# Kernel tuning notes

Hardware: AMD Instinct MI355X
Metric: run time of the kernel (lower is better)

## Reference

```python
import jax, jax.numpy as jnp
import numpy as np

BLOCK_SIZE = 16
MASK_TOKEN_ID = 31999
D_MODEL = 2048
N_HEADS = 16
VOCAB = 32000
NEG = -1e30


def setup_inputs() -> dict:
    key = jax.random.key(0)
    ks = jax.random.split(key, 8)
    B, S, D, V = 1, 1024, D_MODEL, VOCAB
    sd = 1.0 / np.sqrt(D)
    return {
        "input_ids": jax.random.randint(ks[0], (B, S), 0, V),
        "attention_mask": jnp.ones((B, S), dtype=jnp.float32),
        "hidden_states": jax.random.normal(ks[1], (B, S, D), dtype=jnp.float32),
        "loss_mask": jnp.ones((B, S), dtype=jnp.float32),
        "embed_table": jax.random.normal(ks[2], (V, D), dtype=jnp.float32) * 0.02,
        "Wq": jax.random.normal(ks[3], (D, D), dtype=jnp.float32) * sd,
        "Wk": jax.random.normal(ks[4], (D, D), dtype=jnp.float32) * sd,
        "Wv": jax.random.normal(ks[5], (D, D), dtype=jnp.float32) * sd,
        "Wo": jax.random.normal(ks[6], (D, D), dtype=jnp.float32) * sd,
        "lm_head_w": jax.random.normal(ks[7], (D, V), dtype=jnp.float32) * sd,
    }


def reference(input_ids, attention_mask, hidden_states, loss_mask,
              embed_table, Wq, Wk, Wv, Wo, lm_head_w):
    B, S = input_ids.shape
    bs = BLOCK_SIZE
    L = (S // bs) * bs  # effective_len
    input_ids = input_ids[:, :L]
    hidden_states = hidden_states[:, :L, :]
    loss_mask = loss_mask[:, :L]

    positions = jnp.arange(L)
    is_block_start = positions % bs == 0
    block_ids = positions // bs

    # noise input: first token of each block real, rest MASK
    noise_ids = jnp.where(is_block_start[None, :], input_ids, MASK_TOKEN_ID)
    noise_emb = embed_table[noise_ids]  # [B, L, D]

    # [L, 2L] DFlash mask: ctx kv visible if its block < q block; noise kv if same block
    ctx_vis = block_ids[None, :] < block_ids[:, None]
    noise_vis = block_ids[:, None] == block_ids[None, :]
    full_mask = jnp.concatenate([ctx_vis, noise_vis], axis=1)  # [L, 2L] bool

    # draft attention: q from noise tokens, kv over [target_hidden ; noise]
    H = N_HEADS
    hd = hidden_states.shape[-1] // H
    kv_in = jnp.concatenate([hidden_states, noise_emb], axis=1)  # [B, 2L, D]
    q = (noise_emb @ Wq).reshape(B, L, H, hd).transpose(0, 2, 1, 3)      # [B,H,L,hd]
    k = (kv_in @ Wk).reshape(B, 2 * L, H, hd).transpose(0, 2, 1, 3)      # [B,H,2L,hd]
    v = (kv_in @ Wv).reshape(B, 2 * L, H, hd).transpose(0, 2, 1, 3)
    scores = jnp.einsum("bhqd,bhkd->bhqk", q, k) / jnp.sqrt(jnp.float32(hd))
    scores = jnp.where(full_mask[None, None, :, :], scores, NEG)
    attn = jax.nn.softmax(scores, axis=-1)
    ctx = jnp.einsum("bhqk,bhkd->bhqd", attn, v)
    hidden = ctx.transpose(0, 2, 1, 3).reshape(B, L, -1) @ Wo  # [B, L, D]

    logits = hidden @ lm_head_w  # [B, L, V]

    # dflash loss mask: exclude first block and block starts (gamma=None)
    is_first_block = block_ids == 0
    valid = (~is_first_block) & (~is_block_start)
    combined = loss_mask * valid.astype(jnp.float32)  # [B, L]
    active = combined > 1e-6

    logp = jax.nn.log_softmax(logits, axis=-1)
    ce = -jnp.take_along_axis(logp, input_ids[..., None], axis=-1)[..., 0]  # [B, L]
    count = jnp.sum(active.astype(jnp.float32))
    loss = jnp.sum(jnp.where(active, ce, 0.0)) / count

    preds = jnp.argmax(logits, axis=-1)
    correct = jnp.sum(jnp.where(active, (preds == input_ids).astype(jnp.float32), 0.0))
    accuracy = correct / count
    return loss, accuracy
```

## Files before the change

### kernel.cpp

```cpp
#include <hip/hip_runtime.h>

typedef unsigned int uint32;
typedef unsigned short u16;
typedef __attribute__((ext_vector_type(8))) short bf16x8;
typedef __attribute__((ext_vector_type(4))) float f32x4;

__device__ __forceinline__ u16 f2b(float f) {
  uint32 u = __float_as_uint(f);
  u = (u + 0x7fffu + ((u >> 16) & 1u)) >> 16;
  return (u16)u;
}
__device__ __forceinline__ float b2f(u16 h) {
  return __uint_as_float(((uint32)h) << 16);
}
__device__ __forceinline__ void gl_lds16(const void* g, void* l) {
  typedef const __attribute__((address_space(1))) void* gp_t;
  typedef __attribute__((address_space(3))) void* lp_t;
  __builtin_amdgcn_global_load_lds((gp_t)g, (lp_t)l, 16, 0, 0);
}

#define L 1024
#define D 2048
#define NH 16
#define HD 128
#define VOCAB 32000
#define KV 2048
#define MASK_ID 31999

static constexpr long OFF_KV  = 0;
static constexpr long OFF_WTQ = OFF_KV  + 8388608;
static constexpr long OFF_WTK = OFF_WTQ + 8388608;
static constexpr long OFF_WTV = OFF_WTK + 8388608;
static constexpr long OFF_WTO = OFF_WTV + 8388608;
static constexpr long OFF_Q   = OFF_WTO + 8388608;
static constexpr long OFF_K   = OFF_Q   + 4194304;
static constexpr long OFF_VT  = OFF_K   + 8388608;
static constexpr long OFF_SC  = OFF_VT  + 8388608;
static constexpr long OFF_CTX = OFF_SC  + 67108864;
static constexpr long OFF_HID = OFF_CTX + 4194304;
static constexpr long OFF_LMT = OFF_HID + 4194304;
static constexpr long OFF_LOG = OFF_LMT + 131072000;
static constexpr long OFF_ROW = OFF_LOG + 65536000;
static constexpr long WS_NEED = OFF_ROW + 8192;

__global__ __launch_bounds__(256) void prep_kv(const float* __restrict__ hs,
                                               const int* __restrict__ ids,
                                               const float* __restrict__ emb,
                                               u16* __restrict__ kv) {
  int r = blockIdx.x;
  int t = threadIdx.x;
  const float* src;
  if (r < L) {
    src = hs + (long)r * D;
  } else {
    int p = r - L;
    int id = ((p & 15) == 0) ? ids[p] : MASK_ID;
    src = emb + (long)id * D;
  }
  float4 a = *(const float4*)(src + t * 8);
  float4 b = *(const float4*)(src + t * 8 + 4);
  u16* dst = kv + (long)r * D + t * 8;
  ushort4 o0, o1;
  o0.x = f2b(a.x); o0.y = f2b(a.y); o0.z = f2b(a.z); o0.w = f2b(a.w);
  o1.x = f2b(b.x); o1.y = f2b(b.y); o1.z = f2b(b.z); o1.w = f2b(b.w);
  *(ushort4*)dst = o0;
  *(ushort4*)(dst + 4) = o1;
}

__device__ __forceinline__ void transpose_body(const float* __restrict__ W,
                                               u16* __restrict__ WT,
                                               int Kd, int Nd) {
  __shared__ float tile[64][65];
  int n0 = blockIdx.x * 64;
  int k0 = blockIdx.y * 64;
  int t = threadIdx.x;
#pragma unroll
  for (int p = 0; p < 4; ++p) {
    int idx = p * 256 + t;
    int r = idx >> 4;
    int c = (idx & 15) << 2;
    float4 v = *(const float4*)(W + (long)(k0 + r) * Nd + n0 + c);
    tile[r][c] = v.x; tile[r][c + 1] = v.y; tile[r][c + 2] = v.z; tile[r][c + 3] = v.w;
  }
  __syncthreads();
#pragma unroll
  for (int p = 0; p < 4; ++p) {
    int idx = p * 256 + t;
    int rn = idx >> 4;
    int ck = (idx & 15) << 2;
    ushort4 o;
    o.x = f2b(tile[ck][rn]);
    o.y = f2b(tile[ck + 1][rn]);
    o.z = f2b(tile[ck + 2][rn]);
    o.w = f2b(tile[ck + 3][rn]);
    *(ushort4*)(WT + (long)(n0 + rn) * Kd + k0 + ck) = o;
  }
}

__global__ __launch_bounds__(256) void transpose_conv(const float* __restrict__ W,
                                                      u16* __restrict__ WT,
                                                      int Kd, int Nd) {
  transpose_body(W, WT, Kd, Nd);
}

__global__ __launch_bounds__(256) void transpose4(const float* __restrict__ W0, const float* __restrict__ W1,
                                                  const float* __restrict__ W2, const float* __restrict__ W3,
                                                  u16* __restrict__ T0, u16* __restrict__ T1,
                                                  u16* __restrict__ T2, u16* __restrict__ T3) {
  int z = blockIdx.z;
  const float* W = (z == 0) ? W0 : (z == 1) ? W1 : (z == 2) ? W2 : W3;
  u16* T = (z == 0) ? T0 : (z == 1) ? T1 : (z == 2) ? T2 : T3;
  transpose_body(W, T, D, D);
}

#define EPI_PLAIN 0
#define EPI_TRANS 1
#define EPI_SCORES 2
#define EPI_QKV 3

template <int EPI>
__global__ __launch_bounds__(256) void gemm128(const u16* __restrict__ A, int lda, long aHead,
                                               const u16* __restrict__ BT, int ldb, long bHead,
                                               u16* __restrict__ C, int ldc, long cHead,
                                               int Kd,
                                               u16* __restrict__ Cq, u16* __restrict__ Ck,
                                               u16* __restrict__ Cv) {
  if (EPI == EPI_QKV) {
    if (blockIdx.y < 16 && blockIdx.x < 8) return;
  }
  __shared__ __align__(16) char lds[16384];
  char* a_lds = lds;
  char* b_lds = lds + 8192;
  int tid = threadIdx.x;
  int lane = tid & 63;
  int wave = tid >> 6;
  int wr = wave >> 1, wc = wave & 1;
  int h = blockIdx.z;
  long tm = (long)blockIdx.x * 128;
  long tn = (long)blockIdx.y * 128;
  const u16* Ap = A + (long)h * aHead + tm * lda;
  const u16* Bp = BT + (long)h * bHead + tn * ldb;

  int soff = tid * 16;
  int srow = soff >> 6;
  int scol = (soff & 63) >> 1;
  char* aldsb = a_lds + wave * 1024;
  char* bldsb = b_lds + wave * 1024;

  f32x4 acc[4][4];
#pragma unroll
  for (int i = 0; i < 4; ++i)
#pragma unroll
    for (int j = 0; j < 4; ++j) acc[i][j] = (f32x4){0.f, 0.f, 0.f, 0.f};

  for (int k0 = 0; k0 < Kd; k0 += 32) {
#pragma unroll
    for (int r = 0; r < 2; ++r) {
      gl_lds16(Ap + (long)(srow + r * 64) * lda + k0 + scol, aldsb + r * 4096);
      gl_lds16(Bp + (long)(srow + r * 64) * ldb + k0 + scol, bldsb + r * 4096);
    }
    __syncthreads();
    bf16x8 af[4], bfr[4];
    int ka = (lane >> 4) << 4;
#pragma unroll
    for (int mi = 0; mi < 4; ++mi)
      af[mi] = *(const bf16x8*)(a_lds + (wr * 64 + mi * 16 + (lane & 15)) * 64 + ka);
#pragma unroll
    for (int ni = 0; ni < 4; ++ni)
      bfr[ni] = *(const bf16x8*)(b_lds + (wc * 64 + ni * 16 + (lane & 15)) * 64 + ka);
#pragma unroll
    for (int mi = 0; mi < 4; ++mi)
#pragma unroll
      for (int ni = 0; ni < 4; ++ni)
        acc[mi][ni] = __builtin_amdgcn_mfma_f32_16x16x32_bf16(af[mi], bfr[ni], acc[mi][ni], 0, 0, 0);
    __syncthreads();
  }

  long crow0 = tm + wr * 64 + ((lane >> 4) << 2);
  int ccol0 = wc * 64 + (lane & 15);
  u16* Cp = C + (long)h * cHead;
  const float scale = 0.08838834764831845f;
#pragma unroll
  for (int mi = 0; mi < 4; ++mi) {
#pragma unroll
    for (int ni = 0; ni < 4; ++ni) {
      long col = tn + ccol0 + ni * 16;
#pragma unroll
      for (int j = 0; j < 4; ++j) {
        long row = crow0 + mi * 16 + j;
        float v = acc[mi][ni][j];
        if (EPI == EPI_PLAIN) {
          Cp[row * ldc + col] = f2b(v);
        } else if (EPI == EPI_TRANS) {
          Cp[col * ldc + row] = f2b(v);
        } else if (EPI == EPI_SCORES) {
          int rb = (int)row >> 4;
          int cb = (int)col >> 4;
          bool vis = (col < 1024) ? (cb < rb) : ((cb - 64) == rb);
          Cp[row * ldc + col] = f2b(vis ? v * scale : -1e30f);
        } else {
          if (col < 2048) {
            if (row >= 1024) Cq[(row - 1024) * 2048 + col] = f2b(v);
          } else if (col < 4096) {
            Ck[row * 2048 + (col - 2048)] = f2b(v);
          } else {
            Cv[(col - 4096) * 2048 + row] = f2b(v);
          }
        }
      }
    }
  }
}

__global__ __launch_bounds__(512, 2) void gemm256(const u16* __restrict__ A, int lda,
                                                  const u16* __restrict__ BT, int ldb,
                                                  u16* __restrict__ C, int ldc,
                                                  int Kd, int mtiles) {
  __shared__ __align__(16) char lds[131072];
  int nwg = gridDim.x;
  int orig = blockIdx.x;
  int q8 = nwg >> 3, r8 = nwg & 7;
  int xcd = orig & 7, idx = orig >> 3;
  int wg = (xcd < r8 ? xcd * (q8 + 1) : r8 * (q8 + 1) + (xcd - r8) * q8) + idx;
  int tm = wg % mtiles, tn = wg / mtiles;

  int tid = threadIdx.x, lane = tid & 63, w = tid >> 6;
  int wm = w >> 2, wn = w & 3;
  const u16* Ap = A + (long)tm * 256 * lda;
  const u16* Bp = BT + (long)tn * 256 * ldb;
  int NT = Kd >> 6;
  int maxs = NT << 2;

  auto STAGE_SLOT = [&](int s) {
    if (s >= maxs) return;
    int tau = s >> 2, hh = s & 3;
    int kind = (hh & 1) ^ 1;
    int ks = hh >> 1;
    const u16* src = kind ? Bp : Ap;
    int ld = kind ? ldb : lda;
    char* dst0 = lds + (tau & 1) * 65536 + kind * 32768 + ks * 16384;
    long kbase = (long)tau * 64 + ks * 32;
#pragma unroll
    for (int l = 0; l < 2; ++l) {
      int o = tid * 16 + l * 8192;
      int rr = o >> 6;
      int ch = (o >> 4) & 3;
      int clog = ch ^ ((rr >> 1) & 3);
      gl_lds16(src + (long)rr * ld + kbase + clog * 8, dst0 + w * 1024 + l * 8192);
    }
  };
  auto LDA = [&](int tau, int ks, int mi) -> bf16x8 {
    int rr = wm * 128 + mi * 16 + (lane & 15);
    int qq = lane >> 4;
    return *(const bf16x8*)(lds + (tau & 1) * 65536 + ks * 16384 + rr * 64 +
                            ((qq ^ ((rr >> 1) & 3)) << 4));
  };
  auto LDB = [&](int tau, int ks, int ni) -> bf16x8 {
    int rr = wn * 64 + ni * 16 + (lane & 15);
    int qq = lane >> 4;
    return *(const bf16x8*)(lds + (tau & 1) * 65536 + 32768 + ks * 16384 + rr * 64 +
                            ((qq ^ ((rr >> 1) & 3)) << 4));
  };

  f32x4 acc[8][4];
#pragma unroll
  for (int i = 0; i < 8; ++i)
#pragma unroll
    for (int j = 0; j < 4; ++j) acc[i][j] = (f32x4){0.f, 0.f, 0.f, 0.f};

  STAGE_SLOT(0); STAGE_SLOT(1); STAGE_SLOT(2); STAGE_SLOT(3);
  asm volatile("s_waitcnt vmcnt(4)" ::: "memory");
  STAGE_SLOT(4); STAGE_SLOT(5); STAGE_SLOT(6);
  asm volatile("s_waitcnt vmcnt(6)" ::: "memory");
  __builtin_amdgcn_s_barrier();
  __builtin_amdgcn_sched_barrier(0);

  bf16x8 bfr[4];

#define G256_PHASE(TAU, KS, MH, SLOT, WAITV)                                   \
  {                                                                            \
    bf16x8 af[4];                                                              \
    if (MH == 0) {                                                             \
      bfr[0] = LDB(TAU, KS, 0); bfr[1] = LDB(TAU, KS, 1);                      \
      bfr[2] = LDB(TAU, KS, 2); bfr[3] = LDB(TAU, KS, 3);                      \
    }                                                                          \
    af[0] = LDA(TAU, KS, MH * 4 + 0); af[1] = LDA(TAU, KS, MH * 4 + 1);        \
    af[2] = LDA(TAU, KS, MH * 4 + 2); af[3] = LDA(TAU, KS, MH * 4 + 3);        \
    STAGE_SLOT(SLOT);                                                          \
    __builtin_amdgcn_sched_barrier(0);                                         \
    __builtin_amdgcn_s_barrier();                                              \
    asm volatile("s_waitcnt lgkmcnt(0)" ::: "memory");                         \
    __builtin_amdgcn_sched_barrier(0);                                         \
    __builtin_amdgcn_s_setprio(1);                                             \
    _Pragma("unroll")                                                          \
    for (int mi2 = 0; mi2 < 4; ++mi2)                                          \
      _Pragma("unroll")                                                        \
      for (int ni = 0; ni < 4; ++ni)                                           \
        acc[MH * 4 + mi2][ni] = __builtin_amdgcn_mfma_f32_16x16x32_bf16(       \
            af[mi2], bfr[ni], acc[MH * 4 + mi2][ni], 0, 0, 0);                 \
    __builtin_amdgcn_s_setprio(0);                                             \
    __builtin_amdgcn_sched_barrier(0);                                         \
    if (WAITV == 6) asm volatile("s_waitcnt vmcnt(6)" ::: "memory");           \
    else if (WAITV == 0) asm volatile("s_waitcnt vmcnt(0)" ::: "memory");      \
    __builtin_amdgcn_s_barrier();                                              \
    __builtin_amdgcn_sched_barrier(0);                                         \
  }

  for (int t = 0; t < NT; t += 2) {
    int s0 = 4 * t;
    int w4 = (t + 2 >= NT) ? 0 : 6;
    G256_PHASE(t,     0, 0, s0 + 7,  -1)
    G256_PHASE(t,     0, 1, s0 + 8,  -1)
    G256_PHASE(t,     1, 0, s0 + 9,  -1)
    G256_PHASE(t,     1, 1, s0 + 10, w4)
    G256_PHASE(t + 1, 0, 0, s0 + 11, -1)
    G256_PHASE(t + 1, 0, 1, s0 + 12, -1)
    G256_PHASE(t + 1, 1, 0, s0 + 13, -1)
    G256_PHASE(t + 1, 1, 1, s0 + 14, 6)
  }
#undef G256_PHASE

  long crow = (long)tm * 256 + wm * 128 + ((lane >> 4) << 2);
  long ccol = (long)tn * 256 + wn * 64 + (lane & 15);
#pragma unroll
  for (int mi = 0; mi < 8; ++mi)
#pragma unroll
    for (int ni = 0; ni < 4; ++ni)
#pragma unroll
      for (int j = 0; j < 4; ++j)
        C[(crow + mi * 16 + j) * ldc + ccol + ni * 16] = f2b(acc[mi][ni][j]);
}

__global__ __launch_bounds__(256) void softmax_rows(u16* __restrict__ sc) {
  long row = blockIdx.x;
  u16* p = sc + row * 2048;
  int t = threadIdx.x;
  bf16x8 v = *(const bf16x8*)(p + t * 8);
  float f[8];
#pragma unroll
  for (int i = 0; i < 8; ++i) f[i] = b2f((u16)v[i]);
  float m = f[0];
#pragma unroll
  for (int i = 1; i < 8; ++i) m = fmaxf(m, f[i]);
  for (int off = 1; off < 64; off <<= 1) m = fmaxf(m, __shfl_xor(m, off));
  __shared__ float redm[4], reds[4];
  if ((t & 63) == 0) redm[t >> 6] = m;
  __syncthreads();
  m = fmaxf(fmaxf(redm[0], redm[1]), fmaxf(redm[2], redm[3]));
  float e[8];
  float s = 0.f;
#pragma unroll
  for (int i = 0; i < 8; ++i) { e[i] = __expf(f[i] - m); s += e[i]; }
  for (int off = 1; off < 64; off <<= 1) s += __shfl_xor(s, off);
  if ((t & 63) == 0) reds[t >> 6] = s;
  __syncthreads();
  s = reds[0] + reds[1] + reds[2] + reds[3];
  float inv = 1.f / s;
  bf16x8 o;
#pragma unroll
  for (int i = 0; i < 8; ++i) o[i] = (short)f2b(e[i] * inv);
  *(bf16x8*)(p + t * 8) = o;
}

__global__ __launch_bounds__(256) void row_ce(const u16* __restrict__ logits,
                                              const int* __restrict__ ids,
                                              float* __restrict__ rowbuf) {
  int row = blockIdx.x;
  const u16* p = logits + (long)row * VOCAB;
  int t = threadIdx.x;
  int lane = t & 63, w = t >> 6;
  float m = -1e30f;
  int am = VOCAB;
  for (int i = t * 8; i < VOCAB; i += 2048) {
    bf16x8 v = *(const bf16x8*)(p + i);
#pragma unroll
    for (int j = 0; j < 8; ++j) {
      float f = b2f((u16)v[j]);
      if (f > m) { m = f; am = i + j; }
      else if (f == m && (i + j) < am) am = i + j;
    }
  }
  for (int off = 1; off < 64; off <<= 1) {
    float om = __shfl_xor(m, off);
    int oa = __shfl_xor(am, off);
    if (om > m || (om == m && oa < am)) { m = om; am = oa; }
  }
  __shared__ float smax[4]; __shared__ int sidx[4]; __shared__ float ssum[4];
  if (lane == 0) { smax[w] = m; sidx[w] = am; }
  __syncthreads();
  float gm = smax[0]; int gi = sidx[0];
#pragma unroll
  for (int q = 1; q < 4; ++q) {
    if (smax[q] > gm || (smax[q] == gm && sidx[q] < gi)) { gm = smax[q]; gi = sidx[q]; }
  }
  float s = 0.f;
  for (int i = t * 8; i < VOCAB; i += 2048) {
    bf16x8 v = *(const bf16x8*)(p + i);
#pragma unroll
    for (int j = 0; j < 8; ++j) s += __expf(b2f((u16)v[j]) - gm);
  }
  for (int off = 1; off < 64; off <<= 1) s += __shfl_xor(s, off);
  if (lane == 0) ssum[w] = s;
  __syncthreads();
  if (t == 0) {
    float gs = ssum[0] + ssum[1] + ssum[2] + ssum[3];
    int tgt = ids[row];
    float tl = b2f(p[tgt]);
    rowbuf[row * 2] = gm + logf(gs) - tl;
    rowbuf[row * 2 + 1] = (gi == tgt) ? 1.f : 0.f;
  }
}

__global__ __launch_bounds__(256) void final_reduce(const float* __restrict__ rowbuf,
                                                    const float* __restrict__ loss_mask,
                                                    float* __restrict__ out) {
  int t = threadIdx.x;
  float ce = 0.f, cnt = 0.f, cor = 0.f;
  for (int r = t; r < L; r += 256) {
    bool valid = (r >= 16) && ((r & 15) != 0);
    float comb = loss_mask[r] * (valid ? 1.f : 0.f);
    if (comb > 1e-6f) {
      ce += rowbuf[r * 2];
      cor += rowbuf[r * 2 + 1];
      cnt += 1.f;
    }
  }
  for (int off = 1; off < 64; off <<= 1) {
    ce += __shfl_xor(ce, off);
    cnt += __shfl_xor(cnt, off);
    cor += __shfl_xor(cor, off);
  }
  __shared__ float s1[4], s2[4], s3[4];
  int lane = t & 63, w = t >> 6;
  if (lane == 0) { s1[w] = ce; s2[w] = cnt; s3[w] = cor; }
  __syncthreads();
  if (t == 0) {
    float C = s1[0] + s1[1] + s1[2] + s1[3];
    float N = s2[0] + s2[1] + s2[2] + s2[3];
    float R = s3[0] + s3[1] + s3[2] + s3[3];
    out[0] = C / N;
    out[1] = R / N;
  }
}

__global__ void ws_too_small(float* out, float mb) {
  if (threadIdx.x == 0) { out[0] = 1e6f + mb; out[1] = -1e6f; }
}

extern "C" void kernel_launch(void* const* d_in, const int* in_sizes, int n_in,
                              void* d_out, int out_size, void* d_ws, size_t ws_size,
                              hipStream_t stream) {
  const int* ids = (const int*)d_in[0];
  const float* hs = (const float*)d_in[2];
  const float* lmask = (const float*)d_in[3];
  const float* emb = (const float*)d_in[4];
  const float* Wq = (const float*)d_in[5];
  const float* Wk = (const float*)d_in[6];
  const float* Wv = (const float*)d_in[7];
  const float* Wo = (const float*)d_in[8];
  const float* Wlm = (const float*)d_in[9];
  float* out = (float*)d_out;
  char* ws = (char*)d_ws;

  if (ws_size < (size_t)WS_NEED) {
    ws_too_small<<<1, 64, 0, stream>>>(out, (float)(ws_size >> 20));
    return;
  }

  u16* kv  = (u16*)(ws + OFF_KV);
  u16* wtq = (u16*)(ws + OFF_WTQ);
  u16* wtk = (u16*)(ws + OFF_WTK);
  u16* wtv = (u16*)(ws + OFF_WTV);
  u16* wto = (u16*)(ws + OFF_WTO);
  u16* qb  = (u16*)(ws + OFF_Q);
  u16* kb  = (u16*)(ws + OFF_K);
  u16* vt  = (u16*)(ws + OFF_VT);
  u16* sc  = (u16*)(ws + OFF_SC);
  u16* ctx = (u16*)(ws + OFF_CTX);
  u16* hid = (u16*)(ws + OFF_HID);
  u16* lmt = (u16*)(ws + OFF_LMT);
  u16* lgt = (u16*)(ws + OFF_LOG);
  float* rowbuf = (float*)(ws + OFF_ROW);

  prep_kv<<<2048, 256, 0, stream>>>(hs, ids, emb, kv);
  transpose4<<<dim3(32, 32, 4), 256, 0, stream>>>(Wq, Wk, Wv, Wo, wtq, wtk, wtv, wto);
  transpose_conv<<<dim3(500, 32), 256, 0, stream>>>(Wlm, lmt, D, VOCAB);

  gemm128<EPI_QKV><<<dim3(16, 48, 1), 256, 0, stream>>>(kv, D, 0, wtq, D, 0,
                                                        nullptr, 0, 0, D, qb, kb, vt);

  gemm128<EPI_SCORES><<<dim3(8, 16, NH), 256, 0, stream>>>(qb, D, HD, kb, D, HD, sc, KV,
                                                           (long)L * KV, HD,
                                                           nullptr, nullptr, nullptr);
  softmax_rows<<<NH * L, 256, 0, stream>>>(sc);
  gemm128<EPI_PLAIN><<<dim3(8, 1, NH), 256, 0, stream>>>(sc, KV, (long)L * KV, vt, KV,
                                                         (long)HD * KV, ctx, D, HD, KV,
                                                         nullptr, nullptr, nullptr);
  gemm128<EPI_PLAIN><<<dim3(8, 16, 1), 256, 0, stream>>>(ctx, D, 0, wto, D, 0, hid, D, 0, D,
                                                         nullptr, nullptr, nullptr);
  gemm256<<<dim3(500), 512, 0, stream>>>(hid, D, lmt, D, lgt, VOCAB, D, 4);

  row_ce<<<1024, 256, 0, stream>>>(lgt, ids, rowbuf);
  final_reduce<<<1, 256, 0, stream>>>(rowbuf, lmask, out);
}
```

Before: 473.8 us.

## Replace dense score/softmax/PV attention with block-sparse flash kernel; move QKV to gemm256

Replaces the three-kernel attention path (masked scores GEMM writing a full L x 2L bf16 matrix, row softmax, PV GEMM) with one flash-style kernel. Each wave handles one 16-row query block and visits only the visible key blocks (earlier context blocks plus its own noise block), using an online softmax. This removes the score matrix round trip and the masked work. The QKV projection also moves from the 128-tile GEMM to the 256-tile pipelined GEMM, with a custom tile map that skips the unused Q rows. The flash kernel loads K and V fragments straight from global memory, and its wave work is uneven because the number of visible blocks grows with the block index.

```diff
diff --git a/kernel.cpp b/kernel.cpp
--- a/kernel.cpp
+++ b/kernel.cpp
@@ -114,20 +114,13 @@
 }
 
 #define EPI_PLAIN 0
-#define EPI_TRANS 1
-#define EPI_SCORES 2
 #define EPI_QKV 3
 
 template <int EPI>
 __global__ __launch_bounds__(256) void gemm128(const u16* __restrict__ A, int lda, long aHead,
                                                const u16* __restrict__ BT, int ldb, long bHead,
                                                u16* __restrict__ C, int ldc, long cHead,
-                                               int Kd,
-                                               u16* __restrict__ Cq, u16* __restrict__ Ck,
-                                               u16* __restrict__ Cv) {
-  if (EPI == EPI_QKV) {
-    if (blockIdx.y < 16 && blockIdx.x < 8) return;
-  }
+                                               int Kd) {
   __shared__ __align__(16) char lds[16384];
   char* a_lds = lds;
   char* b_lds = lds + 8192;
@@ -179,7 +172,6 @@
   long crow0 = tm + wr * 64 + ((lane >> 4) << 2);
   int ccol0 = wc * 64 + (lane & 15);
   u16* Cp = C + (long)h * cHead;
-  const float scale = 0.08838834764831845f;
 #pragma unroll
   for (int mi = 0; mi < 4; ++mi) {
 #pragma unroll
@@ -188,41 +180,32 @@
 #pragma unroll
       for (int j = 0; j < 4; ++j) {
         long row = crow0 + mi * 16 + j;
-        float v = acc[mi][ni][j];
-        if (EPI == EPI_PLAIN) {
-          Cp[row * ldc + col] = f2b(v);
-        } else if (EPI == EPI_TRANS) {
-          Cp[col * ldc + row] = f2b(v);
-        } else if (EPI == EPI_SCORES) {
-          int rb = (int)row >> 4;
-          int cb = (int)col >> 4;
-          bool vis = (col < 1024) ? (cb < rb) : ((cb - 64) == rb);
-          Cp[row * ldc + col] = f2b(vis ? v * scale : -1e30f);
-        } else {
-          if (col < 2048) {
-            if (row >= 1024) Cq[(row - 1024) * 2048 + col] = f2b(v);
-          } else if (col < 4096) {
-            Ck[row * 2048 + (col - 2048)] = f2b(v);
-          } else {
-            Cv[(col - 4096) * 2048 + row] = f2b(v);
-          }
-        }
+        Cp[row * ldc + col] = f2b(acc[mi][ni][j]);
       }
     }
   }
 }
 
+template <int EPI>
 __global__ __launch_bounds__(512, 2) void gemm256(const u16* __restrict__ A, int lda,
                                                   const u16* __restrict__ BT, int ldb,
                                                   u16* __restrict__ C, int ldc,
-                                                  int Kd, int mtiles) {
+                                                  int Kd, int mtiles,
+                                                  u16* __restrict__ Cq, u16* __restrict__ Ck,
+                                                  u16* __restrict__ Cv) {
   __shared__ __align__(16) char lds[131072];
   int nwg = gridDim.x;
   int orig = blockIdx.x;
   int q8 = nwg >> 3, r8 = nwg & 7;
   int xcd = orig & 7, idx = orig >> 3;
   int wg = (xcd < r8 ? xcd * (q8 + 1) : r8 * (q8 + 1) + (xcd - r8) * q8) + idx;
-  int tm = wg % mtiles, tn = wg / mtiles;
+  int tm, tn;
+  if (EPI == EPI_QKV) {
+    if (wg < 32) { tn = wg >> 2; tm = 4 + (wg & 3); }
+    else { int e = wg - 32; tn = 8 + (e >> 3); tm = e & 7; }
+  } else {
+    tm = wg % mtiles; tn = wg / mtiles;
+  }
 
   int tid = threadIdx.x, lane = tid & 63, w = tid >> 6;
   int wm = w >> 2, wn = w & 3;
@@ -327,39 +310,129 @@
 #pragma unroll
     for (int ni = 0; ni < 4; ++ni)
 #pragma unroll
-      for (int j = 0; j < 4; ++j)
-        C[(crow + mi * 16 + j) * ldc + ccol + ni * 16] = f2b(acc[mi][ni][j]);
-}
-
-__global__ __launch_bounds__(256) void softmax_rows(u16* __restrict__ sc) {
-  long row = blockIdx.x;
-  u16* p = sc + row * 2048;
-  int t = threadIdx.x;
-  bf16x8 v = *(const bf16x8*)(p + t * 8);
-  float f[8];
-#pragma unroll
-  for (int i = 0; i < 8; ++i) f[i] = b2f((u16)v[i]);
-  float m = f[0];
-#pragma unroll
-  for (int i = 1; i < 8; ++i) m = fmaxf(m, f[i]);
-  for (int off = 1; off < 64; off <<= 1) m = fmaxf(m, __shfl_xor(m, off));
-  __shared__ float redm[4], reds[4];
-  if ((t & 63) == 0) redm[t >> 6] = m;
-  __syncthreads();
-  m = fmaxf(fmaxf(redm[0], redm[1]), fmaxf(redm[2], redm[3]));
-  float e[8];
-  float s = 0.f;
-#pragma unroll
-  for (int i = 0; i < 8; ++i) { e[i] = __expf(f[i] - m); s += e[i]; }
-  for (int off = 1; off < 64; off <<= 1) s += __shfl_xor(s, off);
-  if ((t & 63) == 0) reds[t >> 6] = s;
-  __syncthreads();
-  s = reds[0] + reds[1] + reds[2] + reds[3];
-  float inv = 1.f / s;
-  bf16x8 o;
-#pragma unroll
-  for (int i = 0; i < 8; ++i) o[i] = (short)f2b(e[i] * inv);
-  *(bf16x8*)(p + t * 8) = o;
+      for (int j = 0; j < 4; ++j) {
+        long row = crow + mi * 16 + j;
+        long col = ccol + ni * 16;
+        u16 val = f2b(acc[mi][ni][j]);
+        if (EPI == EPI_PLAIN) {
+          C[row * ldc + col] = val;
+        } else {
+          if (col < 2048) {
+            if (row >= 1024) Cq[(row - 1024) * D + col] = val;
+          } else if (col < 4096) {
+            Ck[row * D + (col - 2048)] = val;
+          } else {
+            Cv[(col - 4096) * KV + row] = val;
+          }
+        }
+      }
+}
+
+__global__ __launch_bounds__(256) void flash_attn(const u16* __restrict__ qb,
+                                                  const u16* __restrict__ kb,
+                                                  const u16* __restrict__ vt,
+                                                  u16* __restrict__ ctx) {
+  int tid = threadIdx.x;
+  int lane = tid & 63;
+  int wid = blockIdx.x * 4 + (tid >> 6);
+  int h = wid >> 6;
+  int rb = wid & 63;
+  int lq = lane & 15;
+  int g = lane >> 4;
+  const float scale = 0.08838834764831845f;
+
+  const u16* qrow = qb + (long)(rb * 16 + lq) * D + h * HD + g * 8;
+  bf16x8 qf[4];
+#pragma unroll
+  for (int c = 0; c < 4; ++c) qf[c] = *(const bf16x8*)(qrow + c * 32);
+
+  f32x4 o[8];
+#pragma unroll
+  for (int i = 0; i < 8; ++i) o[i] = (f32x4){0.f, 0.f, 0.f, 0.f};
+  float m = -1e30f, lsum = 0.f;
+
+  int nb = rb + 1;
+  for (int bp = 0; bp < nb; bp += 2) {
+    bool validB = (bp + 1) < nb;
+    int tokA = (bp < rb) ? bp * 16 : 1024 + rb * 16;
+    int bB = bp + 1;
+    int tokB = validB ? ((bB < rb) ? bB * 16 : 1024 + rb * 16) : tokA;
+
+    f32x4 sA = (f32x4){0.f, 0.f, 0.f, 0.f};
+    f32x4 sB = (f32x4){0.f, 0.f, 0.f, 0.f};
+    const u16* ka = kb + (long)(tokA + lq) * D + h * HD + g * 8;
+#pragma unroll
+    for (int c = 0; c < 4; ++c) {
+      bf16x8 kf = *(const bf16x8*)(ka + c * 32);
+      sA = __builtin_amdgcn_mfma_f32_16x16x32_bf16(kf, qf[c], sA, 0, 0, 0);
+    }
+    if (validB) {
+      const u16* kbp = kb + (long)(tokB + lq) * D + h * HD + g * 8;
+#pragma unroll
+      for (int c = 0; c < 4; ++c) {
+        bf16x8 kf = *(const bf16x8*)(kbp + c * 32);
+        sB = __builtin_amdgcn_mfma_f32_16x16x32_bf16(kf, qf[c], sB, 0, 0, 0);
+      }
+    }
+
+    float s8[8];
+#pragma unroll
+    for (int j = 0; j < 4; ++j) s8[j] = sA[j] * scale;
+#pragma unroll
+    for (int j = 0; j < 4; ++j) s8[4 + j] = validB ? sB[j] * scale : -1e30f;
+    float mx = s8[0];
+#pragma unroll
+    for (int j = 1; j < 8; ++j) mx = fmaxf(mx, s8[j]);
+    mx = fmaxf(mx, __shfl_xor(mx, 16));
+    mx = fmaxf(mx, __shfl_xor(mx, 32));
+    float mn = fmaxf(m, mx);
+    float sc_f = __expf(m - mn);
+    m = mn;
+    float p[8], ps = 0.f;
+#pragma unroll
+    for (int j = 0; j < 8; ++j) { p[j] = __expf(s8[j] - mn); ps += p[j]; }
+    ps += __shfl_xor(ps, 16);
+    ps += __shfl_xor(ps, 32);
+    lsum = lsum * sc_f + ps;
+
+    uint32 Aw0 = (uint32)f2b(p[0]) | ((uint32)f2b(p[1]) << 16);
+    uint32 Aw1 = (uint32)f2b(p[2]) | ((uint32)f2b(p[3]) << 16);
+    uint32 Bw0 = (uint32)f2b(p[4]) | ((uint32)f2b(p[5]) << 16);
+    uint32 Bw1 = (uint32)f2b(p[6]) | ((uint32)f2b(p[7]) << 16);
+    int s0 = (((2 * g) & 3) << 4) + lq;
+    int s1 = (((2 * g + 1) & 3) << 4) + lq;
+    uint32 a00 = (uint32)__shfl((int)Aw0, s0), a01 = (uint32)__shfl((int)Aw1, s0);
+    uint32 a10 = (uint32)__shfl((int)Aw0, s1), a11 = (uint32)__shfl((int)Aw1, s1);
+    uint32 b00 = (uint32)__shfl((int)Bw0, s0), b01 = (uint32)__shfl((int)Bw1, s0);
+    uint32 b10 = (uint32)__shfl((int)Bw0, s1), b11 = (uint32)__shfl((int)Bw1, s1);
+    union { uint32 u[4]; bf16x8 v; } pu;
+    pu.u[0] = (g < 2) ? a00 : b00;
+    pu.u[1] = (g < 2) ? a01 : b01;
+    pu.u[2] = (g < 2) ? a10 : b10;
+    pu.u[3] = (g < 2) ? a11 : b11;
+
+#pragma unroll
+    for (int nt = 0; nt < 8; ++nt)
+#pragma unroll
+      for (int j = 0; j < 4; ++j) o[nt][j] *= sc_f;
+    int tok_g = (g < 2) ? (tokA + g * 8) : (tokB + (g - 2) * 8);
+    const u16* vrow = vt + (long)(h * HD + lq) * KV + tok_g;
+#pragma unroll
+    for (int nt = 0; nt < 8; ++nt) {
+      bf16x8 vf = *(const bf16x8*)(vrow + (long)nt * 16 * KV);
+      o[nt] = __builtin_amdgcn_mfma_f32_16x16x32_bf16(vf, pu.v, o[nt], 0, 0, 0);
+    }
+  }
+
+  float inv = 1.f / lsum;
+  u16* cp = ctx + (long)(rb * 16 + lq) * D + h * HD + g * 4;
+#pragma unroll
+  for (int nt = 0; nt < 8; ++nt) {
+    ushort4 st;
+    st.x = f2b(o[nt][0] * inv); st.y = f2b(o[nt][1] * inv);
+    st.z = f2b(o[nt][2] * inv); st.w = f2b(o[nt][3] * inv);
+    *(ushort4*)(cp + nt * 16) = st;
+  }
 }
 
 __global__ __launch_bounds__(256) void row_ce(const u16* __restrict__ logits,
@@ -475,7 +548,6 @@
   u16* qb  = (u16*)(ws + OFF_Q);
   u16* kb  = (u16*)(ws + OFF_K);
   u16* vt  = (u16*)(ws + OFF_VT);
-  u16* sc  = (u16*)(ws + OFF_SC);
   u16* ctx = (u16*)(ws + OFF_CTX);
   u16* hid = (u16*)(ws + OFF_HID);
   u16* lmt = (u16*)(ws + OFF_LMT);
@@ -486,19 +558,14 @@
   transpose4<<<dim3(32, 32, 4), 256, 0, stream>>>(Wq, Wk, Wv, Wo, wtq, wtk, wtv, wto);
   transpose_conv<<<dim3(500, 32), 256, 0, stream>>>(Wlm, lmt, D, VOCAB);
 
-  gemm128<EPI_QKV><<<dim3(16, 48, 1), 256, 0, stream>>>(kv, D, 0, wtq, D, 0,
-                                                        nullptr, 0, 0, D, qb, kb, vt);
-
-  gemm128<EPI_SCORES><<<dim3(8, 16, NH), 256, 0, stream>>>(qb, D, HD, kb, D, HD, sc, KV,
-                                                           (long)L * KV, HD,
-                                                           nullptr, nullptr, nullptr);
-  softmax_rows<<<NH * L, 256, 0, stream>>>(sc);
-  gemm128<EPI_PLAIN><<<dim3(8, 1, NH), 256, 0, stream>>>(sc, KV, (long)L * KV, vt, KV,
-                                                         (long)HD * KV, ctx, D, HD, KV,
-                                                         nullptr, nullptr, nullptr);
-  gemm128<EPI_PLAIN><<<dim3(8, 16, 1), 256, 0, stream>>>(ctx, D, 0, wto, D, 0, hid, D, 0, D,
-                                                         nullptr, nullptr, nullptr);
-  gemm256<<<dim3(500), 512, 0, stream>>>(hid, D, lmt, D, lgt, VOCAB, D, 4);
+  gemm256<EPI_QKV><<<dim3(160), 512, 0, stream>>>(kv, D, wtq, D, nullptr, 0, D, 0,
+                                                  qb, kb, vt);
+
+  flash_attn<<<dim3(256), 256, 0, stream>>>(qb, kb, vt, ctx);
+
+  gemm128<EPI_PLAIN><<<dim3(8, 16, 1), 256, 0, stream>>>(ctx, D, 0, wto, D, 0, hid, D, 0, D);
+  gemm256<EPI_PLAIN><<<dim3(500), 512, 0, stream>>>(hid, D, lmt, D, lgt, VOCAB, D, 4,
+                                                    nullptr, nullptr, nullptr);
 
   row_ce<<<1024, 256, 0, stream>>>(lgt, ids, rowbuf);
   final_reduce<<<1, 256, 0, stream>>>(rowbuf, lmask, out);
```

Measured after the change: 458.5 us. 1.03x faster.
